# Kernel optimization log

Measured on AMD Instinct MI355X. Metric: run time of the kernel, lower is better.

Reference implementation:

```python
import jax, jax.numpy as jnp
import numpy as np

B, T_HIST, T_FC, C, F_IN, HID = 64, 24, 48, 4096, 8, 64
OUT = 1
IN_DEC = 3  # decoder consumes last 3 features of X


def setup_inputs() -> dict:
    key = jax.random.key(0)
    ks = jax.random.split(key, 12)
    s_in = 1.0 / np.sqrt(IN_DEC + OUT)
    s_h = 1.0 / np.sqrt(HID)
    return {
        "X": jax.random.normal(ks[0], (B, T_HIST + T_FC, C, F_IN), jnp.float32),
        "H": jax.random.normal(ks[1], (B, C, HID), jnp.float32),
        "xn": jax.random.normal(ks[2], (B, C, OUT), jnp.float32),
        # fc_in: Linear(in_dim+out_dim -> hid)
        "W_in": jax.random.uniform(ks[3], (HID, IN_DEC + OUT), jnp.float32, -s_in, s_in),
        "b_in": jax.random.uniform(ks[4], (HID,), jnp.float32, -s_in, s_in),
        # GRUCell(hid, hid): gates ordered (r, z, n) as in torch
        "W_ih": jax.random.uniform(ks[5], (3 * HID, HID), jnp.float32, -s_h, s_h),
        "W_hh": jax.random.uniform(ks[6], (3 * HID, HID), jnp.float32, -s_h, s_h),
        "b_ih": jax.random.uniform(ks[7], (3 * HID,), jnp.float32, -s_h, s_h),
        "b_hh": jax.random.uniform(ks[8], (3 * HID,), jnp.float32, -s_h, s_h),
        # fc_out: Linear(hid -> 1)
        "W_out": jax.random.uniform(ks[9], (OUT, HID), jnp.float32, -s_h, s_h),
        "b_out": jax.random.uniform(ks[10], (OUT,), jnp.float32, -s_h, s_h),
    }


def reference(X, H, xn, W_in, b_in, W_ih, W_hh, b_ih, b_hh, W_out, b_out):
    # exogenous decoder inputs: [T_FC, B, C, 3]
    Xs = jnp.transpose(X[:, T_HIST:T_HIST + T_FC, :, -IN_DEC:], (1, 0, 2, 3))
    h0 = H.reshape(B * C, HID)

    def step(carry, xt):
        h, x_prev = carry  # h: [B*C, HID], x_prev: [B, C, 1]
        x = jnp.concatenate([x_prev, xt], axis=-1).reshape(B * C, IN_DEC + OUT)
        x = x @ W_in.T + b_in                      # fc_in
        gi = x @ W_ih.T + b_ih                     # [B*C, 3*HID]
        gh = h @ W_hh.T + b_hh
        i_r, i_z, i_n = jnp.split(gi, 3, axis=-1)
        h_r, h_z, h_n = jnp.split(gh, 3, axis=-1)
        r = jax.nn.sigmoid(i_r + h_r)
        z = jax.nn.sigmoid(i_z + h_z)
        n = jnp.tanh(i_n + r * h_n)
        h_new = (1.0 - z) * n + z * h
        x_out = h_new.reshape(B, C, HID) @ W_out.T + b_out  # [B, C, 1]
        return (h_new, x_out), x_out

    _, preds = jax.lax.scan(step, (h0, xn), Xs)   # preds: [T_FC, B, C, 1]
    return jnp.transpose(preds, (1, 0, 2, 3))      # [B, T_FC, C, 1]
```

## Files before the change

kernel.cpp:

```cpp
#include <hip/hip_runtime.h>

#define B_    64
#define C_    4096
#define T_ALL 72
#define T_H   24
#define T_FC  48
#define F_IN  8
#define HID   64
#define NSEQ  (B_ * C_)

__global__ __launch_bounds__(192) void setup_kernel(
    const float* __restrict__ W_in, const float* __restrict__ b_in,
    const float* __restrict__ W_ih, const float* __restrict__ b_ih,
    float* __restrict__ ws) {
  int j = threadIdx.x;
  float a0 = 0.f, a1 = 0.f, a2 = 0.f, a3 = 0.f, ab = 0.f;
  for (int k = 0; k < HID; ++k) {
    float w = W_ih[j * HID + k];
    a0 += w * W_in[k * 4 + 0];
    a1 += w * W_in[k * 4 + 1];
    a2 += w * W_in[k * 4 + 2];
    a3 += w * W_in[k * 4 + 3];
    ab += w * b_in[k];
  }
  ws[j * 4 + 0] = a0;
  ws[j * 4 + 1] = a1;
  ws[j * 4 + 2] = a2;
  ws[j * 4 + 3] = a3;
  ws[768 + j] = ab + b_ih[j];
}

__device__ __forceinline__ float fast_sigmoid(float x) {
  float e = __builtin_amdgcn_exp2f(-1.4426950408889634f * x);
  return __builtin_amdgcn_rcpf(1.0f + e);
}
__device__ __forceinline__ float fast_tanh(float x) {
  float e = __builtin_amdgcn_exp2f(-2.8853900817779268f * x);
  return 2.0f * __builtin_amdgcn_rcpf(1.0f + e) - 1.0f;
}

__global__ __launch_bounds__(256, 2) void gru_kernel(
    const float* __restrict__ X, const float* __restrict__ H,
    const float* __restrict__ xn, const float* __restrict__ W_hh,
    const float* __restrict__ b_hh, const float* __restrict__ W_out,
    const float* __restrict__ b_out, const float* __restrict__ ws,
    float* __restrict__ out) {
  __shared__ float sW[192 * 64];
  __shared__ float sWc[192 * 4];
  __shared__ float sbc[192];
  __shared__ float sbh[192];
  __shared__ float sWo[64];

  const int tid = threadIdx.x;
  for (int i = tid; i < 192 * 64; i += 256) sW[i] = W_hh[i];
  for (int i = tid; i < 768; i += 256) sWc[i] = ws[i];
  if (tid < 192) {
    sbc[tid] = ws[768 + tid];
    sbh[tid] = b_hh[tid];
  }
  if (tid < 64) sWo[tid] = W_out[tid];
  __syncthreads();

  const int s = blockIdx.x * 256 + tid;
  const int b = s >> 12;
  const int c = s & 4095;

  float h[HID];
  const float4* Hp = reinterpret_cast<const float4*>(H + (size_t)s * HID);
#pragma unroll
  for (int k = 0; k < HID / 4; ++k) {
    float4 v = Hp[k];
    h[4 * k + 0] = v.x;
    h[4 * k + 1] = v.y;
    h[4 * k + 2] = v.z;
    h[4 * k + 3] = v.w;
  }
  float xp = xn[s];

  const float* Xp = X + (((size_t)b * T_ALL + T_H) * C_ + c) * F_IN + 5;
  float* Op = out + (size_t)b * (T_FC * C_) + c;
  const float bo = b_out[0];

  const float4* sW4 = reinterpret_cast<const float4*>(sW);

  float x1 = Xp[0];
  float x2 = Xp[1];
  float x3 = Xp[2];

#pragma unroll 1
  for (int t = 0; t < T_FC; ++t) {
    const float* Xn = Xp + ((t < T_FC - 1) ? (C_ * F_IN) : 0);
    const float p1 = Xn[0];
    const float p2 = Xn[1];
    const float p3 = Xn[2];

    float hn[HID];
    float o = bo;
#pragma unroll
    for (int u = 0; u < HID; ++u) {
      float gr = sbh[u];
      float gz = sbh[64 + u];
      float gn = sbh[128 + u];
#pragma unroll
      for (int k4 = 0; k4 < HID / 4; ++k4) {
        float4 wr = sW4[u * 16 + k4];
        float4 wz = sW4[(64 + u) * 16 + k4];
        float4 wn = sW4[(128 + u) * 16 + k4];
        gr += h[4 * k4 + 0] * wr.x + h[4 * k4 + 1] * wr.y +
              h[4 * k4 + 2] * wr.z + h[4 * k4 + 3] * wr.w;
        gz += h[4 * k4 + 0] * wz.x + h[4 * k4 + 1] * wz.y +
              h[4 * k4 + 2] * wz.z + h[4 * k4 + 3] * wz.w;
        gn += h[4 * k4 + 0] * wn.x + h[4 * k4 + 1] * wn.y +
              h[4 * k4 + 2] * wn.z + h[4 * k4 + 3] * wn.w;
      }
      float ir = sbc[u] + xp * sWc[4 * u + 0] + x1 * sWc[4 * u + 1] +
                 x2 * sWc[4 * u + 2] + x3 * sWc[4 * u + 3];
      float iz = sbc[64 + u] + xp * sWc[4 * (64 + u) + 0] +
                 x1 * sWc[4 * (64 + u) + 1] + x2 * sWc[4 * (64 + u) + 2] +
                 x3 * sWc[4 * (64 + u) + 3];
      float in_ = sbc[128 + u] + xp * sWc[4 * (128 + u) + 0] +
                  x1 * sWc[4 * (128 + u) + 1] + x2 * sWc[4 * (128 + u) + 2] +
                  x3 * sWc[4 * (128 + u) + 3];
      float r = fast_sigmoid(ir + gr);
      float z = fast_sigmoid(iz + gz);
      float n = fast_tanh(in_ + r * gn);
      float hu = (1.0f - z) * n + z * h[u];
      hn[u] = hu;
      o += hu * sWo[u];
    }
#pragma unroll
    for (int k = 0; k < HID; ++k) h[k] = hn[k];
    *Op = o;
    Op += C_;
    xp = o;
    x1 = p1;
    x2 = p2;
    x3 = p3;
    Xp = Xn;
  }
}

extern "C" void kernel_launch(void* const* d_in, const int* in_sizes, int n_in,
                              void* d_out, int out_size, void* d_ws,
                              size_t ws_size, hipStream_t stream) {
  const float* X     = (const float*)d_in[0];
  const float* H     = (const float*)d_in[1];
  const float* xn    = (const float*)d_in[2];
  const float* W_in  = (const float*)d_in[3];
  const float* b_in  = (const float*)d_in[4];
  const float* W_ih  = (const float*)d_in[5];
  const float* W_hh  = (const float*)d_in[6];
  const float* b_ih  = (const float*)d_in[7];
  const float* b_hh  = (const float*)d_in[8];
  const float* W_out = (const float*)d_in[9];
  const float* b_out = (const float*)d_in[10];
  float* out = (float*)d_out;
  float* ws  = (float*)d_ws;

  setup_kernel<<<1, 192, 0, stream>>>(W_in, b_in, W_ih, b_ih, ws);
  gru_kernel<<<NSEQ / 256, 256, 0, stream>>>(X, H, xn, W_hh, b_hh, W_out,
                                             b_out, ws, out);
}
```

Before: 9.939 ms.

## Map one wavefront per sequence with register-resident GRU weights

Each sequence is now handled by one 64-lane wavefront, with one lane per hidden unit, instead of one thread per sequence. Each lane keeps its three W_hh rows (192 floats) and its input-projection coefficients in registers. The hidden state is broadcast through a small per-wave LDS buffer, and the fc_out dot product becomes a cross-lane shuffle reduction. This removes the heavy per-step LDS weight streaming of the old layout. In exchange, every wave reloads all weights from global/L2 at start, register pressure is high, and each wave's X reads are redundant across lanes.

```diff
diff --git a/kernel.cpp b/kernel.cpp
--- a/kernel.cpp
+++ b/kernel.cpp
@@ -39,49 +39,50 @@
   return 2.0f * __builtin_amdgcn_rcpf(1.0f + e) - 1.0f;
 }
 
+#define REP16(M) M(0) M(1) M(2) M(3) M(4) M(5) M(6) M(7) \
+                 M(8) M(9) M(10) M(11) M(12) M(13) M(14) M(15)
+
 __global__ __launch_bounds__(256, 2) void gru_kernel(
     const float* __restrict__ X, const float* __restrict__ H,
     const float* __restrict__ xn, const float* __restrict__ W_hh,
     const float* __restrict__ b_hh, const float* __restrict__ W_out,
     const float* __restrict__ b_out, const float* __restrict__ ws,
     float* __restrict__ out) {
-  __shared__ float sW[192 * 64];
-  __shared__ float sWc[192 * 4];
-  __shared__ float sbc[192];
-  __shared__ float sbh[192];
-  __shared__ float sWo[64];
+  __shared__ float sH[4 * HID];
 
-  const int tid = threadIdx.x;
-  for (int i = tid; i < 192 * 64; i += 256) sW[i] = W_hh[i];
-  for (int i = tid; i < 768; i += 256) sWc[i] = ws[i];
-  if (tid < 192) {
-    sbc[tid] = ws[768 + tid];
-    sbh[tid] = b_hh[tid];
-  }
-  if (tid < 64) sWo[tid] = W_out[tid];
-  __syncthreads();
-
-  const int s = blockIdx.x * 256 + tid;
+  const int tid  = threadIdx.x;
+  const int lane = tid & 63;
+  const int wid  = __builtin_amdgcn_readfirstlane(tid >> 6);
+  const int s = blockIdx.x * 4 + wid;
   const int b = s >> 12;
   const int c = s & 4095;
 
-  float h[HID];
-  const float4* Hp = reinterpret_cast<const float4*>(H + (size_t)s * HID);
-#pragma unroll
-  for (int k = 0; k < HID / 4; ++k) {
-    float4 v = Hp[k];
-    h[4 * k + 0] = v.x;
-    h[4 * k + 1] = v.y;
-    h[4 * k + 2] = v.z;
-    h[4 * k + 3] = v.w;
-  }
+  const float4* Wr4 = reinterpret_cast<const float4*>(W_hh + lane * HID);
+  const float4* Wz4 = reinterpret_cast<const float4*>(W_hh + (64 + lane) * HID);
+  const float4* Wn4 = reinterpret_cast<const float4*>(W_hh + (128 + lane) * HID);
+#define LOADW(i) float4 wr##i = Wr4[i]; float4 wz##i = Wz4[i]; float4 wn##i = Wn4[i];
+  REP16(LOADW)
+#undef LOADW
+
+  const float4* Wc4 = reinterpret_cast<const float4*>(ws);
+  const float4 wcr = Wc4[lane];
+  const float4 wcz = Wc4[64 + lane];
+  const float4 wcn = Wc4[128 + lane];
+  const float br  = ws[768 + lane] + b_hh[lane];
+  const float bz  = ws[832 + lane] + b_hh[64 + lane];
+  const float bcn = ws[896 + lane];
+  const float bhn = b_hh[128 + lane];
+  const float wo  = W_out[lane];
+  const float bo  = b_out[0];
+
+  float h  = H[(size_t)s * HID + lane];
   float xp = xn[s];
 
   const float* Xp = X + (((size_t)b * T_ALL + T_H) * C_ + c) * F_IN + 5;
   float* Op = out + (size_t)b * (T_FC * C_) + c;
-  const float bo = b_out[0];
 
-  const float4* sW4 = reinterpret_cast<const float4*>(sW);
+  float* mysH = sH + wid * HID;
+  const float4* mysH4 = reinterpret_cast<const float4*>(mysH);
 
   float x1 = Xp[0];
   float x2 = Xp[1];
@@ -94,43 +95,35 @@
     const float p2 = Xn[1];
     const float p3 = Xn[2];
 
-    float hn[HID];
-    float o = bo;
-#pragma unroll
-    for (int u = 0; u < HID; ++u) {
-      float gr = sbh[u];
-      float gz = sbh[64 + u];
-      float gn = sbh[128 + u];
-#pragma unroll
-      for (int k4 = 0; k4 < HID / 4; ++k4) {
-        float4 wr = sW4[u * 16 + k4];
-        float4 wz = sW4[(64 + u) * 16 + k4];
-        float4 wn = sW4[(128 + u) * 16 + k4];
-        gr += h[4 * k4 + 0] * wr.x + h[4 * k4 + 1] * wr.y +
-              h[4 * k4 + 2] * wr.z + h[4 * k4 + 3] * wr.w;
-        gz += h[4 * k4 + 0] * wz.x + h[4 * k4 + 1] * wz.y +
-              h[4 * k4 + 2] * wz.z + h[4 * k4 + 3] * wz.w;
-        gn += h[4 * k4 + 0] * wn.x + h[4 * k4 + 1] * wn.y +
-              h[4 * k4 + 2] * wn.z + h[4 * k4 + 3] * wn.w;
-      }
-      float ir = sbc[u] + xp * sWc[4 * u + 0] + x1 * sWc[4 * u + 1] +
-                 x2 * sWc[4 * u + 2] + x3 * sWc[4 * u + 3];
-      float iz = sbc[64 + u] + xp * sWc[4 * (64 + u) + 0] +
-                 x1 * sWc[4 * (64 + u) + 1] + x2 * sWc[4 * (64 + u) + 2] +
-                 x3 * sWc[4 * (64 + u) + 3];
-      float in_ = sbc[128 + u] + xp * sWc[4 * (128 + u) + 0] +
-                  x1 * sWc[4 * (128 + u) + 1] + x2 * sWc[4 * (128 + u) + 2] +
-                  x3 * sWc[4 * (128 + u) + 3];
-      float r = fast_sigmoid(ir + gr);
-      float z = fast_sigmoid(iz + gz);
-      float n = fast_tanh(in_ + r * gn);
-      float hu = (1.0f - z) * n + z * h[u];
-      hn[u] = hu;
-      o += hu * sWo[u];
-    }
-#pragma unroll
-    for (int k = 0; k < HID; ++k) h[k] = hn[k];
-    *Op = o;
+    mysH[lane] = h;
+
+    float gr = br, gz = bz, gn = bhn;
+#define DOT(i) { const float4 hv = mysH4[i];                                   \
+    gr += hv.x * wr##i.x + hv.y * wr##i.y + hv.z * wr##i.z + hv.w * wr##i.w;   \
+    gz += hv.x * wz##i.x + hv.y * wz##i.y + hv.z * wz##i.z + hv.w * wz##i.w;   \
+    gn += hv.x * wn##i.x + hv.y * wn##i.y + hv.z * wn##i.z + hv.w * wn##i.w; }
+    REP16(DOT)
+#undef DOT
+
+    gr += xp * wcr.x + x1 * wcr.y + x2 * wcr.z + x3 * wcr.w;
+    gz += xp * wcz.x + x1 * wcz.y + x2 * wcz.z + x3 * wcz.w;
+    float in_ = bcn + xp * wcn.x + x1 * wcn.y + x2 * wcn.z + x3 * wcn.w;
+
+    const float r = fast_sigmoid(gr);
+    const float z = fast_sigmoid(gz);
+    const float n = fast_tanh(in_ + r * gn);
+    h = (1.0f - z) * n + z * h;
+
+    float po = h * wo;
+    po += __shfl_xor(po, 1, 64);
+    po += __shfl_xor(po, 2, 64);
+    po += __shfl_xor(po, 4, 64);
+    po += __shfl_xor(po, 8, 64);
+    po += __shfl_xor(po, 16, 64);
+    po += __shfl_xor(po, 32, 64);
+    const float o = po + bo;
+
+    if (lane == 0) *Op = o;
     Op += C_;
     xp = o;
     x1 = p1;
@@ -158,6 +151,6 @@
   float* ws  = (float*)d_ws;
 
   setup_kernel<<<1, 192, 0, stream>>>(W_in, b_in, W_ih, b_ih, ws);
-  gru_kernel<<<NSEQ / 256, 256, 0, stream>>>(X, H, xn, W_hh, b_hh, W_out,
-                                             b_out, ws, out);
+  gru_kernel<<<NSEQ / 4, 256, 0, stream>>>(X, H, xn, W_hh, b_hh, W_out,
+                                           b_out, ws, out);
 }
```

Result: faster. 9.516 ms (-4.3%).
